# Optimization experiments

Hardware: AMD Instinct MI355X
Metric: run time of the kernel (lower is better)

The kernel has to match this reference:

```python
import jax, jax.numpy as jnp
import numpy as np

Q = 4096   # query_size = argument_size*relation_size*position_size = 32*16*8
L = 8192   # number of context rows


def setup_inputs() -> dict:
    key = jax.random.key(0)
    k1, k2, k3 = jax.random.split(key, 3)
    query = jax.random.normal(k1, (Q,), dtype=jnp.float32)
    context_vector = jax.random.normal(k2, (L, Q), dtype=jnp.float32)
    # torch Linear(2Q, Q, bias=False): weight shape [Q, 2Q], scaled init
    K_w = jax.random.normal(k3, (Q, 2 * Q), dtype=jnp.float32) / np.sqrt(2 * Q)
    return {"query": query, "context_vector": context_vector, "K_w": K_w}


def reference(query, context_vector, K_w):
    # score[l] = <context_vector[l], query>  -> [L]
    score = context_vector @ query
    attention = jax.nn.softmax(score, axis=0)          # softmax over L
    s_t = attention @ context_vector                    # [Q]
    gamma = jnp.concatenate([query, s_t])               # [2Q]
    return K_w @ gamma                                   # Linear(2Q -> Q), no bias
```

## Files before the change

### kernel.cpp

```cpp
#include <hip/hip_runtime.h>

#define Q 4096
#define L 8192
#define RPB 8
#define NCB (L / RPB)
#define NKW 1024

__global__ __launch_bounds__(256) void k1_kernel(
    const float* __restrict__ qvec, const float* __restrict__ ctx,
    const float* __restrict__ Kw, float* __restrict__ partial,
    float* __restrict__ score, float* __restrict__ out1)
{
    __shared__ float sred[4][RPB];
    const int tid  = threadIdx.x;
    const int lane = tid & 63;
    const int wid  = tid >> 6;

    if (blockIdx.x < NCB) {
        const float4* __restrict__ qg = (const float4*)qvec;
        const float4* __restrict__ cb = (const float4*)ctx;
        const int r0 = blockIdx.x * RPB;

        float4 qr[4];
        #pragma unroll
        for (int k = 0; k < 4; ++k) qr[k] = qg[tid + k * 256];

        float d[RPB];
        #pragma unroll
        for (int r = 0; r < RPB; ++r) {
            float a = 0.f;
            #pragma unroll
            for (int k = 0; k < 4; ++k) {
                float4 v = cb[(size_t)(r0 + r) * (Q / 4) + tid + k * 256];
                a = fmaf(v.x, qr[k].x, a); a = fmaf(v.y, qr[k].y, a);
                a = fmaf(v.z, qr[k].z, a); a = fmaf(v.w, qr[k].w, a);
            }
            d[r] = a;
        }
        #pragma unroll
        for (int r = 0; r < RPB; ++r) {
            float a = d[r];
            #pragma unroll
            for (int off = 32; off > 0; off >>= 1) a += __shfl_down(a, off, 64);
            if (lane == 0) sred[wid][r] = a;
        }
        __syncthreads();

        float s[RPB], mb = -3.4e38f;
        #pragma unroll
        for (int r = 0; r < RPB; ++r) {
            s[r] = sred[0][r] + sred[1][r] + sred[2][r] + sred[3][r];
            mb = fmaxf(mb, s[r]);
        }
        float w[RPB];
        #pragma unroll
        for (int r = 0; r < RPB; ++r) w[r] = __expf(s[r] - mb);
        if (tid < RPB) {
            score[r0 + tid] = sred[0][tid] + sred[1][tid] +
                              sred[2][tid] + sred[3][tid];
        }

        float4 acc[4];
        #pragma unroll
        for (int k = 0; k < 4; ++k) acc[k] = make_float4(0.f, 0.f, 0.f, 0.f);
        #pragma unroll
        for (int r = 0; r < RPB; ++r) {
            const float wr = w[r];
            #pragma unroll
            for (int k = 0; k < 4; ++k) {
                float4 v = cb[(size_t)(r0 + r) * (Q / 4) + tid + k * 256];
                acc[k].x = fmaf(wr, v.x, acc[k].x);
                acc[k].y = fmaf(wr, v.y, acc[k].y);
                acc[k].z = fmaf(wr, v.z, acc[k].z);
                acc[k].w = fmaf(wr, v.w, acc[k].w);
            }
        }
        float4* __restrict__ pb = (float4*)(partial + (size_t)blockIdx.x * Q);
        #pragma unroll
        for (int k = 0; k < 4; ++k) pb[tid + k * 256] = acc[k];
    } else {
        const int i = (blockIdx.x - NCB) * 4 + wid;
        const float4* __restrict__ row = (const float4*)(Kw + (size_t)i * (2 * Q));
        const float4* __restrict__ qg  = (const float4*)qvec;
        float a0 = 0.f, a1 = 0.f, a2 = 0.f, a3 = 0.f;
        #pragma unroll
        for (int c = 0; c < 16; c += 4) {
            float4 x0 = row[(c + 0) * 64 + lane], y0 = qg[(c + 0) * 64 + lane];
            float4 x1 = row[(c + 1) * 64 + lane], y1 = qg[(c + 1) * 64 + lane];
            float4 x2 = row[(c + 2) * 64 + lane], y2 = qg[(c + 2) * 64 + lane];
            float4 x3 = row[(c + 3) * 64 + lane], y3 = qg[(c + 3) * 64 + lane];
            a0 = fmaf(x0.x, y0.x, a0); a0 = fmaf(x0.y, y0.y, a0);
            a0 = fmaf(x0.z, y0.z, a0); a0 = fmaf(x0.w, y0.w, a0);
            a1 = fmaf(x1.x, y1.x, a1); a1 = fmaf(x1.y, y1.y, a1);
            a1 = fmaf(x1.z, y1.z, a1); a1 = fmaf(x1.w, y1.w, a1);
            a2 = fmaf(x2.x, y2.x, a2); a2 = fmaf(x2.y, y2.y, a2);
            a2 = fmaf(x2.z, y2.z, a2); a2 = fmaf(x2.w, y2.w, a2);
            a3 = fmaf(x3.x, y3.x, a3); a3 = fmaf(x3.y, y3.y, a3);
            a3 = fmaf(x3.z, y3.z, a3); a3 = fmaf(x3.w, y3.w, a3);
        }
        float dd = (a0 + a1) + (a2 + a3);
        #pragma unroll
        for (int off = 32; off > 0; off >>= 1) dd += __shfl_down(dd, off, 64);
        if (lane == 0) out1[i] = dd;
    }
}

__global__ __launch_bounds__(256) void k2_kernel(
    const float* __restrict__ partial, const float* __restrict__ score,
    float* __restrict__ s_t)
{
    __shared__ float wb[NCB];
    __shared__ float red[4];
    __shared__ float4 sacc[32][8];
    const int tid  = threadIdx.x;
    const int lane = tid & 63;
    const int wid  = tid >> 6;

    float lm = -3.4e38f;
    for (int i = tid; i < L; i += 256) lm = fmaxf(lm, score[i]);
    #pragma unroll
    for (int off = 32; off > 0; off >>= 1) lm = fmaxf(lm, __shfl_down(lm, off, 64));
    if (lane == 0) red[wid] = lm;
    __syncthreads();
    const float M = fmaxf(fmaxf(red[0], red[1]), fmaxf(red[2], red[3]));
    __syncthreads();

    float lz = 0.f;
    for (int i = tid; i < L; i += 256) lz += __expf(score[i] - M);
    #pragma unroll
    for (int off = 32; off > 0; off >>= 1) lz += __shfl_down(lz, off, 64);
    if (lane == 0) red[wid] = lz;
    __syncthreads();
    const float invZ = 1.f / (red[0] + red[1] + red[2] + red[3]);

    for (int b = tid; b < NCB; b += 256) {
        const float4 sa = ((const float4*)score)[2 * b];
        const float4 sb = ((const float4*)score)[2 * b + 1];
        float m8 = fmaxf(fmaxf(fmaxf(sa.x, sa.y), fmaxf(sa.z, sa.w)),
                         fmaxf(fmaxf(sb.x, sb.y), fmaxf(sb.z, sb.w)));
        wb[b] = __expf(m8 - M);
    }
    __syncthreads();

    const int c  = tid & 7;
    const int g  = tid >> 3;
    const int c4 = blockIdx.x * 8 + c;
    const float4* __restrict__ p = (const float4*)partial;
    float4 acc = make_float4(0.f, 0.f, 0.f, 0.f);
    for (int b = g; b < NCB; b += 32) {
        const float w = wb[b];
        float4 v = p[(size_t)b * (Q / 4) + c4];
        acc.x = fmaf(w, v.x, acc.x); acc.y = fmaf(w, v.y, acc.y);
        acc.z = fmaf(w, v.z, acc.z); acc.w = fmaf(w, v.w, acc.w);
    }
    sacc[g][c] = acc;
    __syncthreads();
    if (g == 0) {
        float4 t = sacc[0][c];
        #pragma unroll
        for (int gg = 1; gg < 32; ++gg) {
            float4 u = sacc[gg][c];
            t.x += u.x; t.y += u.y; t.z += u.z; t.w += u.w;
        }
        t.x *= invZ; t.y *= invZ; t.z *= invZ; t.w *= invZ;
        ((float4*)s_t)[c4] = t;
    }
}

__global__ __launch_bounds__(256) void k3_kernel(
    const float* __restrict__ Kw, const float* __restrict__ s_t,
    const float* __restrict__ out1, float* __restrict__ out)
{
    const int lane = threadIdx.x & 63;
    const int wid  = threadIdx.x >> 6;
    const int i = blockIdx.x * 4 + wid;
    const float4* __restrict__ row = (const float4*)(Kw + (size_t)i * (2 * Q) + Q);
    const float4* __restrict__ sg  = (const float4*)s_t;
    float a0 = 0.f, a1 = 0.f, a2 = 0.f, a3 = 0.f;
    #pragma unroll
    for (int c = 0; c < 16; c += 4) {
        float4 x0 = row[(c + 0) * 64 + lane], y0 = sg[(c + 0) * 64 + lane];
        float4 x1 = row[(c + 1) * 64 + lane], y1 = sg[(c + 1) * 64 + lane];
        float4 x2 = row[(c + 2) * 64 + lane], y2 = sg[(c + 2) * 64 + lane];
        float4 x3 = row[(c + 3) * 64 + lane], y3 = sg[(c + 3) * 64 + lane];
        a0 = fmaf(x0.x, y0.x, a0); a0 = fmaf(x0.y, y0.y, a0);
        a0 = fmaf(x0.z, y0.z, a0); a0 = fmaf(x0.w, y0.w, a0);
        a1 = fmaf(x1.x, y1.x, a1); a1 = fmaf(x1.y, y1.y, a1);
        a1 = fmaf(x1.z, y1.z, a1); a1 = fmaf(x1.w, y1.w, a1);
        a2 = fmaf(x2.x, y2.x, a2); a2 = fmaf(x2.y, y2.y, a2);
        a2 = fmaf(x2.z, y2.z, a2); a2 = fmaf(x2.w, y2.w, a2);
        a3 = fmaf(x3.x, y3.x, a3); a3 = fmaf(x3.y, y3.y, a3);
        a3 = fmaf(x3.z, y3.z, a3); a3 = fmaf(x3.w, y3.w, a3);
    }
    float dd = (a0 + a1) + (a2 + a3);
    #pragma unroll
    for (int off = 32; off > 0; off >>= 1) dd += __shfl_down(dd, off, 64);
    if (lane == 0) out[i] = out1[i] + dd;
}

extern "C" void kernel_launch(void* const* d_in, const int* in_sizes, int n_in,
                              void* d_out, int out_size, void* d_ws, size_t ws_size,
                              hipStream_t stream)
{
    const float* query = (const float*)d_in[0];
    const float* ctx   = (const float*)d_in[1];
    const float* Kw    = (const float*)d_in[2];
    float* out = (float*)d_out;

    float* ws      = (float*)d_ws;
    float* score   = ws;
    float* out1    = ws + L;
    float* s_t     = ws + L + Q;
    float* partial = ws + L + 2 * Q;

    k1_kernel<<<NCB + NKW, 256, 0, stream>>>(query, ctx, Kw, partial, score, out1);
    k2_kernel<<<Q / 4 / 8, 256, 0, stream>>>(partial, score, s_t);
    k3_kernel<<<Q / 4, 256, 0, stream>>>(Kw, s_t, out1, out);
}
```

Baseline: 85.07 us.

## Split score pass and compute global softmax before weighted context accumulation

Moves the score dot products into a separate kernel, then has each accumulation block recompute the global max and normalizer with an online softmax over all scores before weighting its context rows. The final reduction becomes a plain sum of pre-normalized partials. This removes the per-block rescaling and the serial softmax in the reduction kernel. In exchange the context matrix is streamed twice and every block rereads all scores.

Result: slower. 89.65 us (+5.4%).

```diff
diff --git a/kernel.cpp b/kernel.cpp
--- a/kernel.cpp
+++ b/kernel.cpp
@@ -2,69 +2,88 @@
 
 #define Q 4096
 #define L 8192
-#define RPB 8
-#define NCB (L / RPB)
-#define NKW 1024
+#define NWB 1024
+#define RWB (L / NWB)
+#define NKB 1024
+#define NRB 64
 
-__global__ __launch_bounds__(256) void k1_kernel(
+__global__ __launch_bounds__(256) void score_kernel(
+    const float* __restrict__ ctx, const float* __restrict__ q,
+    float* __restrict__ score)
+{
+    const int l = blockIdx.x;
+    const float4* __restrict__ row = (const float4*)(ctx + (size_t)l * Q);
+    const float4* __restrict__ qv  = (const float4*)q;
+
+    float acc = 0.f;
+    #pragma unroll
+    for (int i = threadIdx.x; i < Q / 4; i += 256) {
+        float4 a = row[i];
+        float4 b = qv[i];
+        acc = fmaf(a.x, b.x, acc);
+        acc = fmaf(a.y, b.y, acc);
+        acc = fmaf(a.z, b.z, acc);
+        acc = fmaf(a.w, b.w, acc);
+    }
+    #pragma unroll
+    for (int off = 32; off > 0; off >>= 1) acc += __shfl_down(acc, off, 64);
+
+    __shared__ float red[4];
+    const int lane = threadIdx.x & 63;
+    const int wid  = threadIdx.x >> 6;
+    if (lane == 0) red[wid] = acc;
+    __syncthreads();
+    if (threadIdx.x == 0)
+        score[l] = red[0] + red[1] + red[2] + red[3];
+}
+
+__global__ __launch_bounds__(256) void k2_kernel(
     const float* __restrict__ qvec, const float* __restrict__ ctx,
-    const float* __restrict__ Kw, float* __restrict__ partial,
-    float* __restrict__ score, float* __restrict__ out1)
+    const float* __restrict__ Kw, const float* __restrict__ score,
+    float* __restrict__ partial, float* __restrict__ out1)
 {
-    __shared__ float sred[4][RPB];
     const int tid  = threadIdx.x;
     const int lane = tid & 63;
     const int wid  = tid >> 6;
 
-    if (blockIdx.x < NCB) {
-        const float4* __restrict__ qg = (const float4*)qvec;
-        const float4* __restrict__ cb = (const float4*)ctx;
-        const int r0 = blockIdx.x * RPB;
-
-        float4 qr[4];
-        #pragma unroll
-        for (int k = 0; k < 4; ++k) qr[k] = qg[tid + k * 256];
-
-        float d[RPB];
-        #pragma unroll
-        for (int r = 0; r < RPB; ++r) {
-            float a = 0.f;
-            #pragma unroll
-            for (int k = 0; k < 4; ++k) {
-                float4 v = cb[(size_t)(r0 + r) * (Q / 4) + tid + k * 256];
-                a = fmaf(v.x, qr[k].x, a); a = fmaf(v.y, qr[k].y, a);
-                a = fmaf(v.z, qr[k].z, a); a = fmaf(v.w, qr[k].w, a);
-            }
-            d[r] = a;
+    if (blockIdx.x < NWB) {
+        __shared__ float redm[4], redz[4];
+        float mt = -3.4e38f, zt = 0.f;
+        for (int i = tid; i < L; i += 256) {
+            const float s = score[i];
+            if (s > mt) { zt *= __expf(mt - s); mt = s; }
+            zt += __expf(s - mt);
         }
         #pragma unroll
-        for (int r = 0; r < RPB; ++r) {
-            float a = d[r];
-            #pragma unroll
-            for (int off = 32; off > 0; off >>= 1) a += __shfl_down(a, off, 64);
-            if (lane == 0) sred[wid][r] = a;
+        for (int off = 32; off > 0; off >>= 1) {
+            const float om = __shfl_down(mt, off, 64);
+            const float oz = __shfl_down(zt, off, 64);
+            if (om > mt) { zt = zt * __expf(mt - om) + oz; mt = om; }
+            else         { zt += oz * __expf(om - mt); }
         }
+        if (lane == 0) { redm[wid] = mt; redz[wid] = zt; }
         __syncthreads();
+        float M = redm[0], Zc = redz[0];
+        #pragma unroll
+        for (int wv = 1; wv < 4; ++wv) {
+            const float om = redm[wv], oz = redz[wv];
+            if (om > M) { Zc = Zc * __expf(M - om) + oz; M = om; }
+            else        { Zc += oz * __expf(om - M); }
+        }
+        const float invZ = 1.f / Zc;
 
-        float s[RPB], mb = -3.4e38f;
+        const int r0 = blockIdx.x * RWB;
+        float w[RWB];
         #pragma unroll
-        for (int r = 0; r < RPB; ++r) {
-            s[r] = sred[0][r] + sred[1][r] + sred[2][r] + sred[3][r];
-            mb = fmaxf(mb, s[r]);
-        }
-        float w[RPB];
-        #pragma unroll
-        for (int r = 0; r < RPB; ++r) w[r] = __expf(s[r] - mb);
-        if (tid < RPB) {
-            score[r0 + tid] = sred[0][tid] + sred[1][tid] +
-                              sred[2][tid] + sred[3][tid];
-        }
+        for (int r = 0; r < RWB; ++r)
+            w[r] = __expf(score[r0 + r] - M) * invZ;
 
+        const float4* __restrict__ cb = (const float4*)ctx;
         float4 acc[4];
         #pragma unroll
         for (int k = 0; k < 4; ++k) acc[k] = make_float4(0.f, 0.f, 0.f, 0.f);
         #pragma unroll
-        for (int r = 0; r < RPB; ++r) {
+        for (int r = 0; r < RWB; ++r) {
             const float wr = w[r];
             #pragma unroll
             for (int k = 0; k < 4; ++k) {
@@ -79,7 +98,7 @@
         #pragma unroll
         for (int k = 0; k < 4; ++k) pb[tid + k * 256] = acc[k];
     } else {
-        const int i = (blockIdx.x - NCB) * 4 + wid;
+        const int i = (blockIdx.x - NWB) * 4 + wid;
         const float4* __restrict__ row = (const float4*)(Kw + (size_t)i * (2 * Q));
         const float4* __restrict__ qg  = (const float4*)qvec;
         float a0 = 0.f, a1 = 0.f, a2 = 0.f, a3 = 0.f;
@@ -105,64 +124,29 @@
     }
 }
 
-__global__ __launch_bounds__(256) void k2_kernel(
-    const float* __restrict__ partial, const float* __restrict__ score,
-    float* __restrict__ s_t)
+__global__ __launch_bounds__(256) void reduce_kernel(
+    const float* __restrict__ partial, float* __restrict__ s_t)
 {
-    __shared__ float wb[NCB];
-    __shared__ float red[4];
-    __shared__ float4 sacc[32][8];
-    const int tid  = threadIdx.x;
-    const int lane = tid & 63;
-    const int wid  = tid >> 6;
+    __shared__ float4 sacc[16][16];
+    const int c  = threadIdx.x & 15;
+    const int g  = threadIdx.x >> 4;
+    const int c4 = blockIdx.x * 16 + c;
+    const float4* __restrict__ p = (const float4*)partial;
 
-    float lm = -3.4e38f;
-    for (int i = tid; i < L; i += 256) lm = fmaxf(lm, score[i]);
-    #pragma unroll
-    for (int off = 32; off > 0; off >>= 1) lm = fmaxf(lm, __shfl_down(lm, off, 64));
-    if (lane == 0) red[wid] = lm;
-    __syncthreads();
-    const float M = fmaxf(fmaxf(red[0], red[1]), fmaxf(red[2], red[3]));
-    __syncthreads();
-
-    float lz = 0.f;
-    for (int i = tid; i < L; i += 256) lz += __expf(score[i] - M);
-    #pragma unroll
-    for (int off = 32; off > 0; off >>= 1) lz += __shfl_down(lz, off, 64);
-    if (lane == 0) red[wid] = lz;
-    __syncthreads();
-    const float invZ = 1.f / (red[0] + red[1] + red[2] + red[3]);
-
-    for (int b = tid; b < NCB; b += 256) {
-        const float4 sa = ((const float4*)score)[2 * b];
-        const float4 sb = ((const float4*)score)[2 * b + 1];
-        float m8 = fmaxf(fmaxf(fmaxf(sa.x, sa.y), fmaxf(sa.z, sa.w)),
-                         fmaxf(fmaxf(sb.x, sb.y), fmaxf(sb.z, sb.w)));
-        wb[b] = __expf(m8 - M);
-    }
-    __syncthreads();
-
-    const int c  = tid & 7;
-    const int g  = tid >> 3;
-    const int c4 = blockIdx.x * 8 + c;
-    const float4* __restrict__ p = (const float4*)partial;
     float4 acc = make_float4(0.f, 0.f, 0.f, 0.f);
-    for (int b = g; b < NCB; b += 32) {
-        const float w = wb[b];
+    for (int b = g; b < NWB; b += 16) {
         float4 v = p[(size_t)b * (Q / 4) + c4];
-        acc.x = fmaf(w, v.x, acc.x); acc.y = fmaf(w, v.y, acc.y);
-        acc.z = fmaf(w, v.z, acc.z); acc.w = fmaf(w, v.w, acc.w);
+        acc.x += v.x; acc.y += v.y; acc.z += v.z; acc.w += v.w;
     }
     sacc[g][c] = acc;
     __syncthreads();
     if (g == 0) {
         float4 t = sacc[0][c];
         #pragma unroll
-        for (int gg = 1; gg < 32; ++gg) {
+        for (int gg = 1; gg < 16; ++gg) {
             float4 u = sacc[gg][c];
             t.x += u.x; t.y += u.y; t.z += u.z; t.w += u.w;
         }
-        t.x *= invZ; t.y *= invZ; t.z *= invZ; t.w *= invZ;
         ((float4*)s_t)[c4] = t;
     }
 }
@@ -175,27 +159,18 @@
     const int wid  = threadIdx.x >> 6;
     const int i = blockIdx.x * 4 + wid;
     const float4* __restrict__ row = (const float4*)(Kw + (size_t)i * (2 * Q) + Q);
-    const float4* __restrict__ sg  = (const float4*)s_t;
-    float a0 = 0.f, a1 = 0.f, a2 = 0.f, a3 = 0.f;
+    const float4* __restrict__ sv  = (const float4*)s_t;
+    float a = 0.f;
+    #pragma unroll 4
+    for (int it = 0; it < 16; ++it) {
+        const int idx = it * 64 + lane;
+        float4 x = row[idx], y = sv[idx];
+        a = fmaf(x.x, y.x, a); a = fmaf(x.y, y.y, a);
+        a = fmaf(x.z, y.z, a); a = fmaf(x.w, y.w, a);
+    }
     #pragma unroll
-    for (int c = 0; c < 16; c += 4) {
-        float4 x0 = row[(c + 0) * 64 + lane], y0 = sg[(c + 0) * 64 + lane];
-        float4 x1 = row[(c + 1) * 64 + lane], y1 = sg[(c + 1) * 64 + lane];
-        float4 x2 = row[(c + 2) * 64 + lane], y2 = sg[(c + 2) * 64 + lane];
-        float4 x3 = row[(c + 3) * 64 + lane], y3 = sg[(c + 3) * 64 + lane];
-        a0 = fmaf(x0.x, y0.x, a0); a0 = fmaf(x0.y, y0.y, a0);
-        a0 = fmaf(x0.z, y0.z, a0); a0 = fmaf(x0.w, y0.w, a0);
-        a1 = fmaf(x1.x, y1.x, a1); a1 = fmaf(x1.y, y1.y, a1);
-        a1 = fmaf(x1.z, y1.z, a1); a1 = fmaf(x1.w, y1.w, a1);
-        a2 = fmaf(x2.x, y2.x, a2); a2 = fmaf(x2.y, y2.y, a2);
-        a2 = fmaf(x2.z, y2.z, a2); a2 = fmaf(x2.w, y2.w, a2);
-        a3 = fmaf(x3.x, y3.x, a3); a3 = fmaf(x3.y, y3.y, a3);
-        a3 = fmaf(x3.z, y3.z, a3); a3 = fmaf(x3.w, y3.w, a3);
-    }
-    float dd = (a0 + a1) + (a2 + a3);
-    #pragma unroll
-    for (int off = 32; off > 0; off >>= 1) dd += __shfl_down(dd, off, 64);
-    if (lane == 0) out[i] = out1[i] + dd;
+    for (int off = 32; off > 0; off >>= 1) a += __shfl_down(a, off, 64);
+    if (lane == 0) out[i] = out1[i] + a;
 }
 
 extern "C" void kernel_launch(void* const* d_in, const int* in_sizes, int n_in,
@@ -213,7 +188,8 @@
     float* s_t     = ws + L + Q;
     float* partial = ws + L + 2 * Q;
 
-    k1_kernel<<<NCB + NKW, 256, 0, stream>>>(query, ctx, Kw, partial, score, out1);
-    k2_kernel<<<Q / 4 / 8, 256, 0, stream>>>(partial, score, s_t);
+    score_kernel<<<L, 256, 0, stream>>>(ctx, query, score);
+    k2_kernel<<<NWB + NKB, 256, 0, stream>>>(query, ctx, Kw, score, partial, out1);
+    reduce_kernel<<<NRB, 256, 0, stream>>>(partial, s_t);
     k3_kernel<<<Q / 4, 256, 0, stream>>>(Kw, s_t, out1, out);
 }
```
